# Kernel tuning notes

Measured on AMD Instinct MI355X. Metric: run time of the kernel, lower is better.

## Reference

```python
import jax, jax.numpy as jnp
import numpy as np

EPS = 1e-8
SIGMA_MIN = 1e-4
B, T, C, P = 32, 8192, 64, 168


def setup_inputs() -> dict:
    key = jax.random.key(0)
    k1, k2, k3, k4, k5 = jax.random.split(key, 5)
    x_full = jax.random.normal(k1, (B, T, C), dtype=jnp.float32)
    mask = (jax.random.uniform(k2, (B, T, C)) > 0.2).astype(jnp.float32)
    x = mask * x_full  # observed input with missing positions zeroed
    phase_id = jax.random.randint(k3, (B,), 0, P, dtype=jnp.int64)
    anchor_mu = jax.random.normal(k4, (P, C), dtype=jnp.float32)
    anchor_log_sigma = 0.1 * jax.random.normal(k5, (P, C), dtype=jnp.float32)
    return {
        "x": x,
        "mask": mask,
        "phase_id": phase_id,
        "anchor_mu": anchor_mu,
        "anchor_log_sigma": anchor_log_sigma,
        "tau0_raw": jnp.zeros((1,), dtype=jnp.float32),
        "tau1_raw": jnp.zeros((1,), dtype=jnp.float32),
        "missing_token": jnp.zeros((1, 1, C), dtype=jnp.float32),
    }


def _max_gap_ratio(mask):
    # longest contiguous missing run (channel 0) as fraction of T -> (B,1,1)
    missing = mask[:, :, 0] < 0.5  # (B, T)
    Tlen = missing.shape[1]
    idx = jnp.arange(Tlen)[None, :]  # (1, T)
    # index of most recent observed position (running max), -1 if none yet
    last_obs = jax.lax.associative_scan(jnp.maximum,
                                        jnp.where(missing, -1, idx), axis=1)
    run = jnp.where(missing, idx - last_obs, 0)  # current missing run length
    max_run = run.max(axis=1).astype(jnp.float32)
    return (max_run / Tlen)[:, None, None]


def reference(x, mask, phase_id, anchor_mu, anchor_log_sigma,
              tau0_raw, tau1_raw, missing_token):
    # masked moments over time axis
    mask_sum = jnp.clip(mask.sum(axis=1, keepdims=True), EPS, None)  # (B,1,C)
    mu_obs = (mask * x).sum(axis=1, keepdims=True) / mask_sum
    var_obs = (mask * (x - mu_obs) ** 2).sum(axis=1, keepdims=True) / mask_sum
    sigma_obs = jnp.sqrt(var_obs + EPS)

    # anchor lookup
    mu_ref = anchor_mu[phase_id][:, None, :]              # (B,1,C)
    log_sigma_ref = anchor_log_sigma[phase_id][:, None, :]

    coverage = mask.mean(axis=1, keepdims=True)           # (B,1,C)
    gap_ratio = _max_gap_ratio(mask)                      # (B,1,1)

    tau0 = jax.nn.softplus(tau0_raw)
    tau1 = jax.nn.softplus(tau1_raw)
    w = coverage / (coverage + tau0 + tau1 * gap_ratio + EPS)

    mu = w * mu_obs + (1.0 - w) * mu_ref
    log_sigma = w * jnp.log(sigma_obs + EPS) + (1.0 - w) * log_sigma_ref
    sigma = jnp.clip(jnp.exp(log_sigma), SIGMA_MIN, None)

    z = (x - mu) / sigma
    return mask * z + (1.0 - mask) * missing_token
```

## Files before the change

### kernel.cpp

```cpp
#include <hip/hip_runtime.h>
#include <math.h>

#define B_ 32
#define T_ 8192
#define C_ 64
#define S_ 256
#define L_ 32
#define EPS_ 1e-8f
#define SIGMA_MIN_ 1e-4f

typedef float vfloat4 __attribute__((ext_vector_type(4)));

#define SUM_OFF  0
#define SQ_OFF   524288
#define MS_OFF   1048576
#define GAP_OFF  1572864
#define BITX_OFF 1605632
#define BITY_OFF 1736704
#define BITZ_OFF 1867776
#define BITW_OFF 1998848
#define MU_OFF   2129920
#define INV_OFF  2131968

__device__ inline float4 f4add(float4 a, float4 b) {
    return make_float4(a.x + b.x, a.y + b.y, a.z + b.z, a.w + b.w);
}
__device__ inline float4 f4shfl_xor(float4 v, int m) {
    float4 r;
    r.x = __shfl_xor(v.x, m);
    r.y = __shfl_xor(v.y, m);
    r.z = __shfl_xor(v.z, m);
    r.w = __shfl_xor(v.w, m);
    return r;
}
__device__ inline void merge_lr(int l_pre, int l_suf, int l_best, int l_len,
                                int r_pre, int r_suf, int r_best, int r_len,
                                int& pre, int& suf, int& best, int& len) {
    best = max(max(l_best, r_best), l_suf + r_pre);
    pre  = (l_pre == l_len) ? l_len + r_pre : l_pre;
    suf  = (r_suf == r_len) ? r_len + l_suf : r_suf;
    len  = l_len + r_len;
}

__global__ __launch_bounds__(512) void k1_stats(const float* __restrict__ x,
                                                const float* __restrict__ mask,
                                                float* __restrict__ ws) {
    const int bid = blockIdx.x;
    const int b   = bid >> 8;
    const int s   = bid & (S_ - 1);
    const int tid = threadIdx.x;
    const int cq  = tid & 15;
    const int tr  = tid >> 4;
    const int wv  = tid >> 6;

    const long gi = ((long)b * T_ + (long)s * L_ + tr) * 16 + cq;
    const float4 xv = ((const float4*)x)[gi];
    const float4 mv = ((const float4*)mask)[gi];

    unsigned long long balx = __ballot(mv.x >= 0.5f);
    unsigned long long baly = __ballot(mv.y >= 0.5f);
    unsigned long long balz = __ballot(mv.z >= 0.5f);
    unsigned long long balw = __ballot(mv.w >= 0.5f);
    if ((tid & 63) == 0) {
        const int wi = bid * 8 + wv;
        ((unsigned long long*)(ws + BITX_OFF))[wi] = balx;
        ((unsigned long long*)(ws + BITY_OFF))[wi] = baly;
        ((unsigned long long*)(ws + BITZ_OFF))[wi] = balz;
        ((unsigned long long*)(ws + BITW_OFF))[wi] = balw;
    }

    __shared__ unsigned char misbyte[L_];
    if (cq == 0) misbyte[tr] = (mv.x < 0.5f) ? 1 : 0;

    float4 s1 = xv;
    float4 s2 = make_float4(xv.x * xv.x, xv.y * xv.y, xv.z * xv.z, xv.w * xv.w);
    float4 sm = mv;

    s1 = f4add(s1, f4shfl_xor(s1, 16)); s1 = f4add(s1, f4shfl_xor(s1, 32));
    s2 = f4add(s2, f4shfl_xor(s2, 16)); s2 = f4add(s2, f4shfl_xor(s2, 32));
    sm = f4add(sm, f4shfl_xor(sm, 16)); sm = f4add(sm, f4shfl_xor(sm, 32));

    __shared__ float4 shA[8][16];
    __shared__ float4 shB[8][16];
    __shared__ float4 shC[8][16];
    if ((tid & 63) < 16) { shA[wv][cq] = s1; shB[wv][cq] = s2; shC[wv][cq] = sm; }
    __syncthreads();

    if (tid < 16) {
        float4 a = f4add(f4add(f4add(shA[0][tid], shA[1][tid]), f4add(shA[2][tid], shA[3][tid])),
                         f4add(f4add(shA[4][tid], shA[5][tid]), f4add(shA[6][tid], shA[7][tid])));
        float4 c = f4add(f4add(f4add(shB[0][tid], shB[1][tid]), f4add(shB[2][tid], shB[3][tid])),
                         f4add(f4add(shB[4][tid], shB[5][tid]), f4add(shB[6][tid], shB[7][tid])));
        float4 e = f4add(f4add(f4add(shC[0][tid], shC[1][tid]), f4add(shC[2][tid], shC[3][tid])),
                         f4add(f4add(shC[4][tid], shC[5][tid]), f4add(shC[6][tid], shC[7][tid])));
        ((float4*)(ws + SUM_OFF))[bid * 16 + tid] = a;
        ((float4*)(ws + SQ_OFF ))[bid * 16 + tid] = c;
        ((float4*)(ws + MS_OFF ))[bid * 16 + tid] = e;
    }

    if (tid < 32) {
        const int miss = misbyte[tid];
        unsigned long long bal = __ballot(miss != 0);
        if (tid == 0) {
            unsigned int w = (unsigned int)bal;
            int pre, suf, best;
            if (w == 0xFFFFFFFFu) {
                pre = 32; suf = 32; best = 32;
            } else {
                pre = __builtin_ctz(~w);
                suf = __builtin_clz(~w);
                unsigned int tmp = w; best = 0;
                while (tmp) { tmp &= (tmp << 1); ++best; }
            }
            ((int4*)((int*)(ws + GAP_OFF)))[bid] = make_int4(pre, suf, best, L_);
        }
    }
}

__global__ __launch_bounds__(256) void k2_params(const int*   __restrict__ phase_id,
                                                 const float* __restrict__ anchor_mu,
                                                 const float* __restrict__ anchor_ls,
                                                 const float* __restrict__ tau0_raw,
                                                 const float* __restrict__ tau1_raw,
                                                 float* __restrict__ ws) {
    const int b   = blockIdx.x;
    const int tid = threadIdx.x;
    const int q   = tid & 15;
    const int p   = tid >> 4;

    float4 a1 = make_float4(0.f, 0.f, 0.f, 0.f);
    float4 a2 = make_float4(0.f, 0.f, 0.f, 0.f);
    float4 am = make_float4(0.f, 0.f, 0.f, 0.f);
#pragma unroll
    for (int i = 0; i < 16; ++i) {
        const int idx = (b * S_ + (p + i * 16)) * 16 + q;
        a1 = f4add(a1, ((const float4*)(ws + SUM_OFF))[idx]);
        a2 = f4add(a2, ((const float4*)(ws + SQ_OFF ))[idx]);
        am = f4add(am, ((const float4*)(ws + MS_OFF ))[idx]);
    }

    __shared__ float shf[3][16][64];
    *(float4*)&shf[0][p][q * 4] = a1;
    *(float4*)&shf[1][p][q * 4] = a2;
    *(float4*)&shf[2][p][q * 4] = am;
    __syncthreads();

    if (tid < 64) {
        const int4* gp = (const int4*)((const int*)(ws + GAP_OFF)) + b * S_;
        int pre, suf, best, len;
        {
            int4 t0 = gp[tid * 4];
            pre = t0.x; suf = t0.y; best = t0.z; len = t0.w;
        }
#pragma unroll
        for (int k = 1; k < 4; ++k) {
            int4 r = gp[tid * 4 + k];
            merge_lr(pre, suf, best, len, r.x, r.y, r.z, r.w, pre, suf, best, len);
        }
#pragma unroll
        for (int m = 1; m < 64; m <<= 1) {
            int ppre = __shfl_xor(pre, m);
            int psuf = __shfl_xor(suf, m);
            int pbest = __shfl_xor(best, m);
            int plen = __shfl_xor(len, m);
            if (tid & m)
                merge_lr(ppre, psuf, pbest, plen, pre, suf, best, len,
                         pre, suf, best, len);
            else
                merge_lr(pre, suf, best, len, ppre, psuf, pbest, plen,
                         pre, suf, best, len);
        }
        const float gap = (float)best / (float)T_;

        const int c = tid;
        float sum = 0.f, sq = 0.f, ms = 0.f;
#pragma unroll
        for (int pp = 0; pp < 16; ++pp) {
            sum += shf[0][pp][c];
            sq  += shf[1][pp][c];
            ms  += shf[2][pp][c];
        }

        const float msc    = fmaxf(ms, EPS_);
        const float mu_obs = sum / msc;
        float var = (sq - 2.f * mu_obs * sum + mu_obs * mu_obs * ms) / msc;
        var = fmaxf(var, 0.f);
        const float sigma_obs = sqrtf(var + EPS_);
        const float coverage  = ms / (float)T_;

        const float t0 = log1pf(expf(tau0_raw[0]));
        const float t1 = log1pf(expf(tau1_raw[0]));
        const float w  = coverage / (coverage + t0 + t1 * gap + EPS_);

        const int   pid    = phase_id[b];
        const float mu_ref = anchor_mu[pid * C_ + c];
        const float ls_ref = anchor_ls[pid * C_ + c];

        const float mu = w * mu_obs + (1.f - w) * mu_ref;
        const float ls = w * logf(sigma_obs + EPS_) + (1.f - w) * ls_ref;
        const float sigma = fmaxf(expf(ls), SIGMA_MIN_);

        ws[MU_OFF  + b * C_ + c] = mu;
        ws[INV_OFF + b * C_ + c] = 1.f / sigma;
    }
}

__global__ __launch_bounds__(256) void k3_norm(const float* __restrict__ x,
                                               const float* __restrict__ token,
                                               const float* __restrict__ ws,
                                               float* __restrict__ out) {
    const int gid = blockIdx.x * 256 + threadIdx.x;
    const float4* x4 = (const float4*)x;
    const float4* mu4  = (const float4*)(ws + MU_OFF);
    const float4* inv4 = (const float4*)(ws + INV_OFF);
    const float4* tk4  = (const float4*)token;

    const int b = gid >> 17;
    const int p = b * 16 + (gid & 15);

    const int wi = gid >> 6;
    const int ln = gid & 63;
    const unsigned long long wx = ((const unsigned long long*)(ws + BITX_OFF))[wi];
    const unsigned long long wy = ((const unsigned long long*)(ws + BITY_OFF))[wi];
    const unsigned long long wz = ((const unsigned long long*)(ws + BITZ_OFF))[wi];
    const unsigned long long wwd = ((const unsigned long long*)(ws + BITW_OFF))[wi];

    float4 xv = x4[gid];
    float4 mu = mu4[p];
    float4 iv = inv4[p];
    float4 tk = tk4[gid & 15];

    vfloat4 o;
    o.x = ((wx  >> ln) & 1) ? (xv.x - mu.x) * iv.x : tk.x;
    o.y = ((wy  >> ln) & 1) ? (xv.y - mu.y) * iv.y : tk.y;
    o.z = ((wz  >> ln) & 1) ? (xv.z - mu.z) * iv.z : tk.z;
    o.w = ((wwd >> ln) & 1) ? (xv.w - mu.w) * iv.w : tk.w;

    __builtin_nontemporal_store(o, (vfloat4*)out + gid);
}

extern "C" void kernel_launch(void* const* d_in, const int* in_sizes, int n_in,
                              void* d_out, int out_size, void* d_ws, size_t ws_size,
                              hipStream_t stream) {
    const float* x    = (const float*)d_in[0];
    const float* mask = (const float*)d_in[1];
    const int*   pid  = (const int*)  d_in[2];
    const float* amu  = (const float*)d_in[3];
    const float* als  = (const float*)d_in[4];
    const float* t0   = (const float*)d_in[5];
    const float* t1   = (const float*)d_in[6];
    const float* tok  = (const float*)d_in[7];
    float* out = (float*)d_out;
    float* ws  = (float*)d_ws;

    k1_stats<<<B_ * S_, 512, 0, stream>>>(x, mask, ws);
    k2_params<<<B_, 256, 0, stream>>>(pid, amu, als, t0, t1, ws);
    const int n4 = B_ * T_ * C_ / 4;
    k3_norm<<<n4 / 256, 256, 0, stream>>>(x, tok, ws, out);
}
```

Before: 67.44 us.

## Make k1 one wave per 32-row segment with loop accumulation, interleave mask bits

```diff
diff --git a/kernel.cpp b/kernel.cpp
--- a/kernel.cpp
+++ b/kernel.cpp
@@ -9,16 +9,11 @@
 #define EPS_ 1e-8f
 #define SIGMA_MIN_ 1e-4f
 
-typedef float vfloat4 __attribute__((ext_vector_type(4)));
-
 #define SUM_OFF  0
 #define SQ_OFF   524288
 #define MS_OFF   1048576
 #define GAP_OFF  1572864
-#define BITX_OFF 1605632
-#define BITY_OFF 1736704
-#define BITZ_OFF 1867776
-#define BITW_OFF 1998848
+#define BITS_OFF 1605632
 #define MU_OFF   2129920
 #define INV_OFF  2131968
 
@@ -42,78 +37,74 @@
     len  = l_len + r_len;
 }
 
-__global__ __launch_bounds__(512) void k1_stats(const float* __restrict__ x,
+__global__ __launch_bounds__(256) void k1_stats(const float* __restrict__ x,
                                                 const float* __restrict__ mask,
                                                 float* __restrict__ ws) {
-    const int bid = blockIdx.x;
-    const int b   = bid >> 8;
-    const int s   = bid & (S_ - 1);
-    const int tid = threadIdx.x;
-    const int cq  = tid & 15;
-    const int tr  = tid >> 4;
-    const int wv  = tid >> 6;
-
-    const long gi = ((long)b * T_ + (long)s * L_ + tr) * 16 + cq;
-    const float4 xv = ((const float4*)x)[gi];
-    const float4 mv = ((const float4*)mask)[gi];
-
-    unsigned long long balx = __ballot(mv.x >= 0.5f);
-    unsigned long long baly = __ballot(mv.y >= 0.5f);
-    unsigned long long balz = __ballot(mv.z >= 0.5f);
-    unsigned long long balw = __ballot(mv.w >= 0.5f);
-    if ((tid & 63) == 0) {
-        const int wi = bid * 8 + wv;
-        ((unsigned long long*)(ws + BITX_OFF))[wi] = balx;
-        ((unsigned long long*)(ws + BITY_OFF))[wi] = baly;
-        ((unsigned long long*)(ws + BITZ_OFF))[wi] = balz;
-        ((unsigned long long*)(ws + BITW_OFF))[wi] = balw;
-    }
-
-    __shared__ unsigned char misbyte[L_];
-    if (cq == 0) misbyte[tr] = (mv.x < 0.5f) ? 1 : 0;
-
-    float4 s1 = xv;
-    float4 s2 = make_float4(xv.x * xv.x, xv.y * xv.y, xv.z * xv.z, xv.w * xv.w);
-    float4 sm = mv;
+    const int wv   = threadIdx.x >> 6;
+    const int lane = threadIdx.x & 63;
+    const int gw   = blockIdx.x * 4 + wv;
+    const int cq   = lane & 15;
+
+    const float4* x4 = (const float4*)x;
+    const float4* m4 = (const float4*)mask;
+    unsigned long long* bits = (unsigned long long*)(ws + BITS_OFF);
+    const int base = gw * 512 + lane;
+
+    float4 s1 = make_float4(0.f, 0.f, 0.f, 0.f);
+    float4 s2 = make_float4(0.f, 0.f, 0.f, 0.f);
+    float4 sm = make_float4(0.f, 0.f, 0.f, 0.f);
+    unsigned int missw = 0;
+
+#pragma unroll
+    for (int it = 0; it < 8; ++it) {
+        const float4 xv = x4[base + it * 64];
+        const float4 mv = m4[base + it * 64];
+
+        s1.x += xv.x; s1.y += xv.y; s1.z += xv.z; s1.w += xv.w;
+        s2.x += xv.x * xv.x; s2.y += xv.y * xv.y;
+        s2.z += xv.z * xv.z; s2.w += xv.w * xv.w;
+        sm.x += mv.x; sm.y += mv.y; sm.z += mv.z; sm.w += mv.w;
+
+        unsigned long long obx = __ballot(mv.x >= 0.5f);
+        unsigned long long oby = __ballot(mv.y >= 0.5f);
+        unsigned long long obz = __ballot(mv.z >= 0.5f);
+        unsigned long long obw = __ballot(mv.w >= 0.5f);
+        if (lane < 4) {
+            unsigned long long v = (lane == 0) ? obx : (lane == 1) ? oby
+                                 : (lane == 2) ? obz : obw;
+            bits[(size_t)(gw * 8 + it) * 4 + lane] = v;
+        }
+        const unsigned long long nm = ~obx;
+        const unsigned int nib =
+              (unsigned int)(nm & 1ull)
+            | ((unsigned int)((nm >> 16) & 1ull) << 1)
+            | ((unsigned int)((nm >> 32) & 1ull) << 2)
+            | ((unsigned int)((nm >> 48) & 1ull) << 3);
+        missw |= nib << (it * 4);
+    }
 
     s1 = f4add(s1, f4shfl_xor(s1, 16)); s1 = f4add(s1, f4shfl_xor(s1, 32));
     s2 = f4add(s2, f4shfl_xor(s2, 16)); s2 = f4add(s2, f4shfl_xor(s2, 32));
     sm = f4add(sm, f4shfl_xor(sm, 16)); sm = f4add(sm, f4shfl_xor(sm, 32));
 
-    __shared__ float4 shA[8][16];
-    __shared__ float4 shB[8][16];
-    __shared__ float4 shC[8][16];
-    if ((tid & 63) < 16) { shA[wv][cq] = s1; shB[wv][cq] = s2; shC[wv][cq] = sm; }
-    __syncthreads();
-
-    if (tid < 16) {
-        float4 a = f4add(f4add(f4add(shA[0][tid], shA[1][tid]), f4add(shA[2][tid], shA[3][tid])),
-                         f4add(f4add(shA[4][tid], shA[5][tid]), f4add(shA[6][tid], shA[7][tid])));
-        float4 c = f4add(f4add(f4add(shB[0][tid], shB[1][tid]), f4add(shB[2][tid], shB[3][tid])),
-                         f4add(f4add(shB[4][tid], shB[5][tid]), f4add(shB[6][tid], shB[7][tid])));
-        float4 e = f4add(f4add(f4add(shC[0][tid], shC[1][tid]), f4add(shC[2][tid], shC[3][tid])),
-                         f4add(f4add(shC[4][tid], shC[5][tid]), f4add(shC[6][tid], shC[7][tid])));
-        ((float4*)(ws + SUM_OFF))[bid * 16 + tid] = a;
-        ((float4*)(ws + SQ_OFF ))[bid * 16 + tid] = c;
-        ((float4*)(ws + MS_OFF ))[bid * 16 + tid] = e;
-    }
-
-    if (tid < 32) {
-        const int miss = misbyte[tid];
-        unsigned long long bal = __ballot(miss != 0);
-        if (tid == 0) {
-            unsigned int w = (unsigned int)bal;
-            int pre, suf, best;
-            if (w == 0xFFFFFFFFu) {
-                pre = 32; suf = 32; best = 32;
-            } else {
-                pre = __builtin_ctz(~w);
-                suf = __builtin_clz(~w);
-                unsigned int tmp = w; best = 0;
-                while (tmp) { tmp &= (tmp << 1); ++best; }
-            }
-            ((int4*)((int*)(ws + GAP_OFF)))[bid] = make_int4(pre, suf, best, L_);
-        }
+    if (lane < 16) {
+        ((float4*)(ws + SUM_OFF))[gw * 16 + cq] = s1;
+        ((float4*)(ws + SQ_OFF ))[gw * 16 + cq] = s2;
+        ((float4*)(ws + MS_OFF ))[gw * 16 + cq] = sm;
+    }
+
+    if (lane == 0) {
+        const unsigned int w = missw;
+        int pre, suf, best;
+        if (w == 0xFFFFFFFFu) {
+            pre = 32; suf = 32; best = 32;
+        } else {
+            pre = __builtin_ctz(~w);
+            suf = __builtin_clz(~w);
+            unsigned int tmp = w; best = 0;
+            while (tmp) { tmp &= (tmp << 1); ++best; }
+        }
+        ((int4*)((int*)(ws + GAP_OFF)))[gw] = make_int4(pre, suf, best, L_);
     }
 }
 
@@ -218,25 +209,26 @@
     const int b = gid >> 17;
     const int p = b * 16 + (gid & 15);
 
-    const int wi = gid >> 6;
+    const unsigned long long* bw =
+        (const unsigned long long*)(ws + BITS_OFF) + (size_t)(gid >> 6) * 4;
+    const unsigned long long wx = bw[0];
+    const unsigned long long wy = bw[1];
+    const unsigned long long wz = bw[2];
+    const unsigned long long wwd = bw[3];
     const int ln = gid & 63;
-    const unsigned long long wx = ((const unsigned long long*)(ws + BITX_OFF))[wi];
-    const unsigned long long wy = ((const unsigned long long*)(ws + BITY_OFF))[wi];
-    const unsigned long long wz = ((const unsigned long long*)(ws + BITZ_OFF))[wi];
-    const unsigned long long wwd = ((const unsigned long long*)(ws + BITW_OFF))[wi];
 
     float4 xv = x4[gid];
     float4 mu = mu4[p];
     float4 iv = inv4[p];
     float4 tk = tk4[gid & 15];
 
-    vfloat4 o;
+    float4 o;
     o.x = ((wx  >> ln) & 1) ? (xv.x - mu.x) * iv.x : tk.x;
     o.y = ((wy  >> ln) & 1) ? (xv.y - mu.y) * iv.y : tk.y;
     o.z = ((wz  >> ln) & 1) ? (xv.z - mu.z) * iv.z : tk.z;
     o.w = ((wwd >> ln) & 1) ? (xv.w - mu.w) * iv.w : tk.w;
 
-    __builtin_nontemporal_store(o, (vfloat4*)out + gid);
+    ((float4*)out)[gid] = o;
 }
 
 extern "C" void kernel_launch(void* const* d_in, const int* in_sizes, int n_in,
@@ -253,7 +245,7 @@
     float* out = (float*)d_out;
     float* ws  = (float*)d_ws;
 
-    k1_stats<<<B_ * S_, 512, 0, stream>>>(x, mask, ws);
+    k1_stats<<<B_ * S_ / 4, 256, 0, stream>>>(x, mask, ws);
     k2_params<<<B_, 256, 0, stream>>>(pid, amu, als, t0, t1, ws);
     const int n4 = B_ * T_ * C_ / 4;
     k3_norm<<<n4 / 256, 256, 0, stream>>>(x, tok, ws, out);
```

Measured after the change: 62.41 us. 1.08x faster.
